# Performance work log

Hardware: AMD Instinct MI355X
Metric: run time of the kernel (lower is better)

Reference implementation:

```python
import jax, jax.numpy as jnp
import numpy as np

EPS = 1e-9


def setup_inputs() -> dict:
    key = jax.random.key(0)
    k1, k2, k3, k4 = jax.random.split(key, 4)
    B, N = 8192, 256
    T, Q = 4096, 64
    reprs = jax.random.normal(k1, (B, N), dtype=jnp.float32)
    memory = jax.random.normal(k2, (T, Q, N), dtype=jnp.float32)
    # memory bank rows are kept unit-norm by the module's renormalization
    memory = memory / (jnp.linalg.norm(memory, axis=-1, keepdims=True) + EPS)
    alpha = jax.random.uniform(k3, (Q, 1), dtype=jnp.float32)
    track_idxs = jax.random.randint(k4, (B,), 0, T, dtype=jnp.int64)
    return {"reprs": reprs, "memory": memory, "alpha": alpha, "track_idxs": track_idxs}


def reference(reprs, memory, alpha, track_idxs):
    # Vectorized equivalent of MemoryBank.update (init != 'zeros' branch):
    # per track t present in track_idxs, per slot q:
    #   b* = argmin_{b: track_idxs[b]==t} <memory[t,q], reprs[b]>   (first occurrence)
    #   m  = alpha[q] * memory[t,q] + (1-alpha[q]) * reprs[b*]
    #   memory[t,q] = m / (||m|| + eps)
    B, N = reprs.shape
    T, Q, _ = memory.shape
    tid = track_idxs.astype(jnp.int32)

    # similarity of each detection against its own track's Q slots: [B, Q]
    sim = jnp.einsum('bqn,bn->bq', memory[tid], reprs)

    # segment-min over detections of each track -> [T, Q]
    min_val = jnp.full((T, Q), jnp.inf, dtype=sim.dtype).at[tid].min(sim)
    # first detection index achieving the min (matches torch argmin tie-break)
    b_idx = jnp.arange(B, dtype=jnp.int32)[:, None]                 # [B, 1]
    cand = jnp.where(sim == min_val[tid], b_idx, B)                 # [B, Q]
    chosen = jnp.full((T, Q), B, dtype=jnp.int32).at[tid].min(cand)  # [T, Q]

    present = chosen[:, 0] < B                                       # [T]
    sel = reprs[jnp.minimum(chosen, B - 1)]                          # [T, Q, N]

    upd = memory * alpha + sel * (1.0 - alpha)                       # alpha: [Q,1]
    upd = upd / (jnp.linalg.norm(upd, axis=-1, keepdims=True) + EPS)
    return jnp.where(present[:, None, None], upd, memory)
```

## Files before the change

kernel.cpp:

```cpp
#include <hip/hip_runtime.h>
#include <stdint.h>

#define B_DET 8192
#define N_DIM 256
#define T_TRK 4096
#define Q_SLOT 64
#define MAXD   64
#define EPSF   1e-9f

typedef unsigned long long ull;
typedef float nfloat4 __attribute__((ext_vector_type(4)));

__device__ __forceinline__ uint32_t f32_key(float f) {
    uint32_t u = __float_as_uint(f);
    return (u & 0x80000000u) ? ~u : (u | 0x80000000u);
}
__device__ __forceinline__ float key_inv(uint32_t k) {
    uint32_t u = (k & 0x80000000u) ? (k ^ 0x80000000u) : ~k;
    return __uint_as_float(u);
}

__device__ __forceinline__ void nt_store_f4(float* p, float4 v) {
    nfloat4 nv; nv.x = v.x; nv.y = v.y; nv.z = v.z; nv.w = v.w;
    __builtin_nontemporal_store(nv, reinterpret_cast<nfloat4*>(p));
}

__global__ __launch_bounds__(256)
void build_lists(const int* __restrict__ track_idxs,
                 int* __restrict__ cnt, int* __restrict__ list) {
    const int b = blockIdx.x * 256 + threadIdx.x;
    const int t = track_idxs[b];
    const int slot = atomicAdd(&cnt[t], 1);
    if (slot < MAXD) list[t * MAXD + slot] = b;
}

__global__ __launch_bounds__(256)
void fused_update(const float* __restrict__ reprs,
                  const float* __restrict__ memory,
                  const float* __restrict__ alpha,
                  const int* __restrict__ cnt,
                  const int* __restrict__ list,
                  float* __restrict__ out) {
    const int bid  = blockIdx.x;
    const int swz  = (bid & 7) * (8192 >> 3) + (bid >> 3);
    const int t    = swz >> 1;
    const int wave = threadIdx.x >> 6;
    const int lane = threadIdx.x & 63;
    const int g    = lane >> 4;
    const int cidx = lane & 15;
    const int qbase = (swz & 1) * 32 + wave * 8;
    const size_t tbase = (size_t)t * Q_SLOT * N_DIM;

    int D = cnt[t];
    if (D == 0) {
        const size_t rbase = tbase + (size_t)qbase * N_DIM;
        float4 mm[8];
        #pragma unroll
        for (int s = 0; s < 8; ++s)
            mm[s] = reinterpret_cast<const float4*>(memory + rbase + (size_t)s * N_DIM)[lane];
        #pragma unroll
        for (int s = 0; s < 8; ++s)
            nt_store_f4(out + rbase + (size_t)s * N_DIM + lane * 4, mm[s]);
        return;
    }
    if (D > MAXD) D = MAXD;

    float4 m[2][4];
    #pragma unroll
    for (int i = 0; i < 2; ++i) {
        const float* rp = memory + tbase + (size_t)(qbase + i * 4 + g) * N_DIM;
        #pragma unroll
        for (int c = 0; c < 4; ++c)
            m[i][c] = reinterpret_cast<const float4*>(rp)[cidx + c * 16];
    }

    ull   best[2] = { ~0ULL, ~0ULL };
    float bRn2[2] = { 0.0f, 0.0f };

    int b_cur = list[t * MAXD];
    float4 rc[4];
    {
        const float* rp = reprs + (size_t)b_cur * N_DIM;
        #pragma unroll
        for (int cc = 0; cc < 4; ++cc)
            rc[cc] = reinterpret_cast<const float4*>(rp)[cidx + cc * 16];
    }

    for (int d = 0; d < D; ++d) {
        int b_nxt = 0;
        float4 rn[4];
        if (d + 1 < D) {
            b_nxt = list[t * MAXD + d + 1];
            const float* rp = reprs + (size_t)b_nxt * N_DIM;
            #pragma unroll
            for (int cc = 0; cc < 4; ++cc)
                rn[cc] = reinterpret_cast<const float4*>(rp)[cidx + cc * 16];
        }

        float p0 = 0.0f, p1 = 0.0f, rr = 0.0f;
        #pragma unroll
        for (int cc = 0; cc < 4; ++cc) {
            p0 += m[0][cc].x * rc[cc].x + m[0][cc].y * rc[cc].y
                + m[0][cc].z * rc[cc].z + m[0][cc].w * rc[cc].w;
            p1 += m[1][cc].x * rc[cc].x + m[1][cc].y * rc[cc].y
                + m[1][cc].z * rc[cc].z + m[1][cc].w * rc[cc].w;
            rr += rc[cc].x * rc[cc].x + rc[cc].y * rc[cc].y
                + rc[cc].z * rc[cc].z + rc[cc].w * rc[cc].w;
        }
        #pragma unroll
        for (int o = 8; o >= 1; o >>= 1) {
            p0 += __shfl_xor(p0, o, 64);
            p1 += __shfl_xor(p1, o, 64);
            rr += __shfl_xor(rr, o, 64);
        }

        const uint32_t bd = ((uint32_t)b_cur << 6) | (uint32_t)d;
        const ull k0 = ((ull)f32_key(p0) << 32) | bd;
        const ull k1 = ((ull)f32_key(p1) << 32) | bd;
        if (k0 < best[0]) { best[0] = k0; bRn2[0] = rr; }
        if (k1 < best[1]) { best[1] = k1; bRn2[1] = rr; }

        b_cur = b_nxt;
        #pragma unroll
        for (int cc = 0; cc < 4; ++cc) rc[cc] = rn[cc];
    }

    #pragma unroll
    for (int i = 0; i < 2; ++i) {
        const int q = qbase + i * 4 + g;
        const int   bsel = (int)(((uint32_t)best[i]) >> 6);
        const float dot  = key_inv((uint32_t)(best[i] >> 32));
        const float a    = alpha[q];
        const float na   = 1.0f - a;

        const float* rp = reprs + (size_t)bsel * N_DIM;
        const float nrm2 = a * a + na * na * bRn2[i] + 2.0f * a * na * dot;
        const float sc = 1.0f / (sqrtf(nrm2) + EPSF);

        float* op = out + tbase + (size_t)q * N_DIM;
        #pragma unroll
        for (int cc = 0; cc < 4; ++cc) {
            const float4 r = reinterpret_cast<const float4*>(rp)[cidx + cc * 16];
            float4 u;
            u.x = (a * m[i][cc].x + na * r.x) * sc;
            u.y = (a * m[i][cc].y + na * r.y) * sc;
            u.z = (a * m[i][cc].z + na * r.z) * sc;
            u.w = (a * m[i][cc].w + na * r.w) * sc;
            nt_store_f4(op + (cidx + cc * 16) * 4, u);
        }
    }
}

extern "C" void kernel_launch(void* const* d_in, const int* in_sizes, int n_in,
                              void* d_out, int out_size, void* d_ws, size_t ws_size,
                              hipStream_t stream) {
    const float* reprs      = (const float*)d_in[0];
    const float* memory     = (const float*)d_in[1];
    const float* alpha      = (const float*)d_in[2];
    const int*   track_idxs = (const int*)d_in[3];
    float*       out        = (float*)d_out;

    int* cnt  = (int*)d_ws;
    int* list = (int*)((char*)d_ws + T_TRK * sizeof(int));

    (void)hipMemsetAsync(cnt, 0, T_TRK * sizeof(int), stream);
    build_lists<<<B_DET / 256, 256, 0, stream>>>(track_idxs, cnt, list);
    fused_update<<<T_TRK * 2, 256, 0, stream>>>(reprs, memory, alpha, cnt, list, out);
}
```

Measured before the change: 96.04 us.

## Give each wave 32 slots with double-buffered memory row loads

The grid shrinks from 8192 to 2048 blocks. Each wave now handles a half-track of 32 slots in four 8-slot units instead of one 8-slot unit. The memory rows for the next unit are loaded into a second register buffer while the current unit is processed, so global latency overlaps the dot-product loop. The cost is more registers per thread, possibly lower occupancy, and each wave rereading the same detection reprs four times.

```diff
diff --git a/kernel.cpp b/kernel.cpp
--- a/kernel.cpp
+++ b/kernel.cpp
@@ -6,6 +6,7 @@
 #define T_TRK 4096
 #define Q_SLOT 64
 #define MAXD   64
+#define GRID   2048
 #define EPSF   1e-9f
 
 typedef unsigned long long ull;
@@ -34,50 +35,39 @@
     if (slot < MAXD) list[t * MAXD + slot] = b;
 }
 
-__global__ __launch_bounds__(256)
-void fused_update(const float* __restrict__ reprs,
-                  const float* __restrict__ memory,
-                  const float* __restrict__ alpha,
-                  const int* __restrict__ cnt,
-                  const int* __restrict__ list,
-                  float* __restrict__ out) {
-    const int bid  = blockIdx.x;
-    const int swz  = (bid & 7) * (8192 >> 3) + (bid >> 3);
-    const int t    = swz >> 1;
-    const int wave = threadIdx.x >> 6;
-    const int lane = threadIdx.x & 63;
-    const int g    = lane >> 4;
-    const int cidx = lane & 15;
-    const int qbase = (swz & 1) * 32 + wave * 8;
-    const size_t tbase = (size_t)t * Q_SLOT * N_DIM;
-
-    int D = cnt[t];
-    if (D == 0) {
-        const size_t rbase = tbase + (size_t)qbase * N_DIM;
-        float4 mm[8];
-        #pragma unroll
-        for (int s = 0; s < 8; ++s)
-            mm[s] = reinterpret_cast<const float4*>(memory + rbase + (size_t)s * N_DIM)[lane];
-        #pragma unroll
-        for (int s = 0; s < 8; ++s)
-            nt_store_f4(out + rbase + (size_t)s * N_DIM + lane * 4, mm[s]);
-        return;
-    }
-    if (D > MAXD) D = MAXD;
-
-    float4 m[2][4];
+__device__ __forceinline__ void load_m(const float* __restrict__ memory,
+                                       size_t tbase, int qb, int g, int cidx,
+                                       float4 (&buf)[2][4]) {
     #pragma unroll
     for (int i = 0; i < 2; ++i) {
-        const float* rp = memory + tbase + (size_t)(qbase + i * 4 + g) * N_DIM;
+        const float* rp = memory + tbase + (size_t)(qb + i * 4 + g) * N_DIM;
         #pragma unroll
         for (int c = 0; c < 4; ++c)
-            m[i][c] = reinterpret_cast<const float4*>(rp)[cidx + c * 16];
+            buf[i][c] = reinterpret_cast<const float4*>(rp)[cidx + c * 16];
+    }
+}
+
+__device__ __forceinline__ void process_unit(const float* __restrict__ reprs,
+                                             const float* __restrict__ alpha,
+                                             const int* __restrict__ list_t,
+                                             int D, float* __restrict__ out,
+                                             size_t tbase, int qb, int g, int cidx,
+                                             const float4 (&m)[2][4]) {
+    if (D == 0) {
+        #pragma unroll
+        for (int i = 0; i < 2; ++i) {
+            float* op = out + tbase + (size_t)(qb + i * 4 + g) * N_DIM;
+            #pragma unroll
+            for (int c = 0; c < 4; ++c)
+                nt_store_f4(op + (cidx + c * 16) * 4, m[i][c]);
+        }
+        return;
     }
 
     ull   best[2] = { ~0ULL, ~0ULL };
     float bRn2[2] = { 0.0f, 0.0f };
 
-    int b_cur = list[t * MAXD];
+    int b_cur = list_t[0];
     float4 rc[4];
     {
         const float* rp = reprs + (size_t)b_cur * N_DIM;
@@ -90,7 +80,7 @@
         int b_nxt = 0;
         float4 rn[4];
         if (d + 1 < D) {
-            b_nxt = list[t * MAXD + d + 1];
+            b_nxt = list_t[d + 1];
             const float* rp = reprs + (size_t)b_nxt * N_DIM;
             #pragma unroll
             for (int cc = 0; cc < 4; ++cc)
@@ -127,7 +117,7 @@
 
     #pragma unroll
     for (int i = 0; i < 2; ++i) {
-        const int q = qbase + i * 4 + g;
+        const int q = qb + i * 4 + g;
         const int   bsel = (int)(((uint32_t)best[i]) >> 6);
         const float dot  = key_inv((uint32_t)(best[i] >> 32));
         const float a    = alpha[q];
@@ -151,6 +141,39 @@
     }
 }
 
+__global__ __launch_bounds__(256)
+void fused_update(const float* __restrict__ reprs,
+                  const float* __restrict__ memory,
+                  const float* __restrict__ alpha,
+                  const int* __restrict__ cnt,
+                  const int* __restrict__ list,
+                  float* __restrict__ out) {
+    const int bid  = blockIdx.x;
+    const int swb  = (bid & 7) * (GRID >> 3) + (bid >> 3);
+    const int w    = swb * 4 + (threadIdx.x >> 6);
+    const int t    = w >> 1;
+    const int half = w & 1;
+    const int lane = threadIdx.x & 63;
+    const int g    = lane >> 4;
+    const int cidx = lane & 15;
+    const int qb0  = half * 32;
+    const size_t tbase = (size_t)t * Q_SLOT * N_DIM;
+
+    int D = cnt[t];
+    if (D > MAXD) D = MAXD;
+    const int* list_t = list + t * MAXD;
+
+    float4 mA[2][4], mB[2][4];
+    load_m(memory, tbase, qb0 + 0, g, cidx, mA);
+    load_m(memory, tbase, qb0 + 8, g, cidx, mB);
+    process_unit(reprs, alpha, list_t, D, out, tbase, qb0 + 0,  g, cidx, mA);
+    load_m(memory, tbase, qb0 + 16, g, cidx, mA);
+    process_unit(reprs, alpha, list_t, D, out, tbase, qb0 + 8,  g, cidx, mB);
+    load_m(memory, tbase, qb0 + 24, g, cidx, mB);
+    process_unit(reprs, alpha, list_t, D, out, tbase, qb0 + 16, g, cidx, mA);
+    process_unit(reprs, alpha, list_t, D, out, tbase, qb0 + 24, g, cidx, mB);
+}
+
 extern "C" void kernel_launch(void* const* d_in, const int* in_sizes, int n_in,
                               void* d_out, int out_size, void* d_ws, size_t ws_size,
                               hipStream_t stream) {
@@ -165,5 +188,5 @@
 
     (void)hipMemsetAsync(cnt, 0, T_TRK * sizeof(int), stream);
     build_lists<<<B_DET / 256, 256, 0, stream>>>(track_idxs, cnt, list);
-    fused_update<<<T_TRK * 2, 256, 0, stream>>>(reprs, memory, alpha, cnt, list, out);
+    fused_update<<<GRID, 256, 0, stream>>>(reprs, memory, alpha, cnt, list, out);
 }
```

Measured after the change: 113.4 us. 18.1% more time.
